# Kernel tuning notes

Measured on AMD Instinct MI355X. Metric: run time of the kernel, lower is better.

The kernel has to match this reference:

```python
import jax, jax.numpy as jnp
import numpy as np

NEG_SLOPE = 0.2


def gat_layer(x, W, a_src, a_dst, b, src, dst, num_nodes, heads, out_c, concat):
    # Linear transform per head: [N, heads, out_c]
    h = (x @ W).reshape(num_nodes, heads, out_c)
    # Per-node attention logits for source/dest roles: [N, heads]
    e_src = jnp.einsum('nhc,hc->nh', h, a_src)
    e_dst = jnp.einsum('nhc,hc->nh', h, a_dst)
    # Edge-wise scores (gather), LeakyReLU: [E, heads]
    e = jax.nn.leaky_relu(e_src[src] + e_dst[dst], negative_slope=NEG_SLOPE)
    # Segment softmax over incoming edges of each destination node
    m = jax.ops.segment_max(e, dst, num_segments=num_nodes)
    ex = jnp.exp(e - m[dst])
    denom = jax.ops.segment_sum(ex, dst, num_segments=num_nodes)
    alpha = ex / denom[dst]                       # [E, heads]
    # Weighted scatter-aggregate of source messages: [N, heads, out_c]
    out = jax.ops.segment_sum(h[src] * alpha[:, :, None], dst, num_segments=num_nodes)
    if concat:
        out = out.reshape(num_nodes, heads * out_c)
    else:
        out = out.mean(axis=1)
    return out + b


def setup_inputs() -> dict:
    key = jax.random.key(0)
    ks = jax.random.split(key, 12)
    N, E = 50000, 800000
    in_c, out_c, heads = 128, 32, 4
    x = jax.random.normal(ks[0], (N, in_c), dtype=jnp.float32)
    edge_index = jax.random.randint(ks[1], (2, E), 0, N, dtype=jnp.int64)
    s1 = 1.0 / np.sqrt(in_c)
    W1 = jax.random.normal(ks[2], (in_c, heads * out_c), dtype=jnp.float32) * s1
    a_src1 = jax.random.normal(ks[3], (heads, out_c), dtype=jnp.float32) * 0.1
    a_dst1 = jax.random.normal(ks[4], (heads, out_c), dtype=jnp.float32) * 0.1
    b1 = jnp.zeros((heads * out_c,), dtype=jnp.float32)
    s2 = 1.0 / np.sqrt(heads * out_c)
    W2 = jax.random.normal(ks[5], (heads * out_c, out_c), dtype=jnp.float32) * s2
    a_src2 = jax.random.normal(ks[6], (1, out_c), dtype=jnp.float32) * 0.1
    a_dst2 = jax.random.normal(ks[7], (1, out_c), dtype=jnp.float32) * 0.1
    b2 = jnp.zeros((out_c,), dtype=jnp.float32)
    return {"x": x, "edge_index": edge_index, "W1": W1, "a_src1": a_src1,
            "a_dst1": a_dst1, "b1": b1, "W2": W2, "a_src2": a_src2,
            "a_dst2": a_dst2, "b2": b2}


def reference(x, edge_index, W1, a_src1, a_dst1, b1, W2, a_src2, a_dst2, b2):
    N = x.shape[0]
    heads, out_c = a_src1.shape
    # add_self_loops=True (PyG default)
    loops = jnp.arange(N, dtype=edge_index.dtype)
    src = jnp.concatenate([edge_index[0], loops])
    dst = jnp.concatenate([edge_index[1], loops])
    h1 = gat_layer(x, W1, a_src1, a_dst1, b1, src, dst, N, heads, out_c, concat=True)
    h1 = jax.nn.elu(h1)
    out = gat_layer(h1, W2, a_src2, a_dst2, b2, src, dst, N, 1, out_c, concat=False)
    return out
```

## Files before the change

### kernel.cpp

```cpp
#include <hip/hip_runtime.h>
#include <hip/hip_bf16.h>

#define LRELU_SLOPE 0.2f
#define NB_SHIFT 7
#define NBLK 512

typedef __attribute__((ext_vector_type(8))) short short8;
typedef __attribute__((ext_vector_type(4))) float float4v;

__device__ inline float b2f(unsigned short u) {
    union { unsigned int i; float f; } v; v.i = ((unsigned int)u) << 16; return v.f;
}
__device__ inline unsigned short f2b(float f) {
    union { float f; unsigned int i; } v; v.f = f;
    unsigned int x = v.i;
    unsigned int r = x + 0x7fffu + ((x >> 16) & 1u);
    return (unsigned short)(r >> 16);
}
__device__ inline float lrelu(float x) { return x > 0.f ? x : LRELU_SLOPE * x; }

__global__ __launch_bounds__(256) void gemm1_mfma_kernel(
        const float* __restrict__ x, const float* __restrict__ W1,
        const float* __restrict__ a_src, const float* __restrict__ a_dst,
        unsigned short* __restrict__ h1b, float* __restrict__ es,
        float* __restrict__ ed, int N,
        const int* __restrict__ dst, int E, int Etot, int nb, int chunk,
        int* __restrict__ cnt) {
    __shared__ unsigned short xs[64][136];
    __shared__ unsigned short wt[128][136];
    int tid = threadIdx.x;
    int n0 = blockIdx.x * 64;

    for (int i = tid; i < 128 * 128; i += 256) {
        int k = i >> 7, n = i & 127;
        wt[n][k] = f2b(W1[i]);
    }
    {
        int rows = N - n0; if (rows > 64) rows = 64;
        const float4* xv = (const float4*)(x + (size_t)n0 * 128);
        int lim = rows * 32;
        for (int i = tid; i < lim; i += 256) {
            float4 v = xv[i];
            int r = i >> 5, c4 = (i & 31) << 2;
            uint2 p;
            p.x = (unsigned int)f2b(v.x) | ((unsigned int)f2b(v.y) << 16);
            p.y = (unsigned int)f2b(v.z) | ((unsigned int)f2b(v.w) << 16);
            *(uint2*)&xs[r][c4] = p;
        }
    }
    __syncthreads();

    int wave = tid >> 6;
    int lane = tid & 63;
    int lrow = lane & 15;
    int quad = lane >> 4;

    short8 afr[4];
#pragma unroll
    for (int kc = 0; kc < 4; kc++)
        afr[kc] = *(const short8*)&xs[wave * 16 + lrow][kc * 32 + quad * 8];
    __syncthreads();

#pragma unroll
    for (int ct = 0; ct < 8; ct++) {
        float4v acc = {0.f, 0.f, 0.f, 0.f};
#pragma unroll
        for (int kc = 0; kc < 4; kc++) {
            short8 bfr = *(const short8*)&wt[ct * 16 + lrow][kc * 32 + quad * 8];
            acc = __builtin_amdgcn_mfma_f32_16x16x32_bf16(afr[kc], bfr, acc, 0, 0, 0);
        }
#pragma unroll
        for (int r = 0; r < 4; r++) {
            int lr = wave * 16 + quad * 4 + r;
            int grow = n0 + lr;
            unsigned short hb = f2b(acc[r]);
            xs[lr][ct * 16 + lrow] = hb;
            if (grow < N)
                h1b[grow * 128 + ct * 16 + lrow] = hb;
        }
    }
    __syncthreads();

    int row = tid >> 2, h = tid & 3;
    int rg = n0 + row;
    if (rg < N) {
        const float* ap = a_src + h * 32;
        const float* bp = a_dst + h * 32;
        float s = 0.f, d = 0.f;
#pragma unroll
        for (int c2 = 0; c2 < 16; c2++) {
            unsigned int u = *(const unsigned int*)&xs[row][h * 32 + 2 * c2];
            float v0 = b2f((unsigned short)(u & 0xffffu));
            float v1 = b2f((unsigned short)(u >> 16));
            float2 a = *(const float2*)&ap[2 * c2];
            float2 b = *(const float2*)&bp[2 * c2];
            s += v0 * a.x + v1 * a.y;
            d += v0 * b.x + v1 * b.y;
        }
        es[rg * 4 + h] = s;
        ed[rg * 4 + h] = d;
    }

    int* histm = (int*)&wt[0][0];
    int blk = blockIdx.x;
    if (blk < NBLK)
        for (int i = tid; i < nb; i += 256) histm[i] = 0;
    __syncthreads();
    if (blk < NBLK) {
        int lo = blk * chunk;
        int hi = lo + chunk; if (hi > Etot) hi = Etot;
        for (int i = lo + tid; i < hi; i += 256) {
            int d = (i < E) ? dst[i] : (i - E);
            atomicAdd(&histm[d >> NB_SHIFT], 1);
        }
    }
    __syncthreads();
    if (blk < NBLK)
        for (int b = tid; b < nb; b += 256)
            cnt[b * NBLK + blk] = histm[b];
}

__global__ __launch_bounds__(1024) void scanA_kernel(int* cnt, int* bsum, int M) {
    __shared__ int tile[1024];
    int i = blockIdx.x * 1024 + threadIdx.x;
    int v = (i < M) ? cnt[i] : 0;
    tile[threadIdx.x] = v;
    __syncthreads();
    for (int off = 1; off < 1024; off <<= 1) {
        int t = (threadIdx.x >= (unsigned)off) ? tile[threadIdx.x - off] : 0;
        __syncthreads();
        tile[threadIdx.x] += t;
        __syncthreads();
    }
    int incl = tile[threadIdx.x];
    if (i < M) cnt[i] = incl - v;
    if (threadIdx.x == 1023) bsum[blockIdx.x] = incl;
}

__global__ __launch_bounds__(256) void scanB_kernel(int* __restrict__ bsum, int nb) {
    __shared__ int tile[256];
    int v = (threadIdx.x < (unsigned)nb) ? bsum[threadIdx.x] : 0;
    tile[threadIdx.x] = v;
    __syncthreads();
    for (int off = 1; off < 256; off <<= 1) {
        int t = (threadIdx.x >= (unsigned)off) ? tile[threadIdx.x - off] : 0;
        __syncthreads();
        tile[threadIdx.x] += t;
        __syncthreads();
    }
    if (threadIdx.x < (unsigned)nb) bsum[threadIdx.x] = tile[threadIdx.x] - v;
}

__global__ __launch_bounds__(256) void partition_kernel(
        const int* __restrict__ src, const int* __restrict__ dst,
        int E, int Etot, int nb, int chunk,
        const int* __restrict__ cnt, const int* __restrict__ boff,
        int2* __restrict__ bkt) {
    __shared__ int cur[512];
    int blk = blockIdx.x;
    for (int b = threadIdx.x; b < nb; b += 256) {
        int idx = b * NBLK + blk;
        cur[b] = cnt[idx] + boff[idx >> 10];
    }
    __syncthreads();
    int lo = blk * chunk;
    int hi = lo + chunk; if (hi > Etot) hi = Etot;
    for (int i = lo + threadIdx.x; i < hi; i += 256) {
        int s, d;
        if (i < E) { s = src[i]; d = dst[i]; }
        else       { s = d = i - E; }
        int pos = atomicAdd(&cur[d >> NB_SHIFT], 1);
        bkt[pos] = make_int2(s, d);
    }
}

__global__ __launch_bounds__(256) void finalize_kernel(
        const int2* __restrict__ bkt, const int* __restrict__ cnt,
        const int* __restrict__ boff, int nb,
        const float* __restrict__ es, const float* __restrict__ ed,
        int* __restrict__ ptr, int* __restrict__ csr_src,
        _Float16* __restrict__ w1h, int N, int Etot) {
    __shared__ int deg[128];
    __shared__ int scn[128];
    __shared__ int cur[128];
    int b = blockIdx.x;
    int idx0 = b * NBLK;
    int base = cnt[idx0] + boff[idx0 >> 10];
    int nextbase;
    if (b + 1 < nb) {
        int idx1 = (b + 1) * NBLK;
        nextbase = cnt[idx1] + boff[idx1 >> 10];
    } else nextbase = Etot;
    int count = nextbase - base;
    int node0 = b << NB_SHIFT;
    int nodes = N - node0; if (nodes > 128) nodes = 128;

    if (threadIdx.x < 128) deg[threadIdx.x] = 0;
    __syncthreads();
    for (int i = threadIdx.x; i < count; i += 256)
        atomicAdd(&deg[bkt[base + i].y - node0], 1);
    __syncthreads();
    int v = (threadIdx.x < 128) ? deg[threadIdx.x] : 0;
    if (threadIdx.x < 128) scn[threadIdx.x] = v;
    __syncthreads();
    for (int off = 1; off < 128; off <<= 1) {
        int t = (threadIdx.x < 128 && threadIdx.x >= (unsigned)off) ? scn[threadIdx.x - off] : 0;
        __syncthreads();
        if (threadIdx.x < 128) scn[threadIdx.x] += t;
        __syncthreads();
    }
    if (threadIdx.x < 128) {
        int excl = scn[threadIdx.x] - v;
        cur[threadIdx.x] = excl;
        if (threadIdx.x < nodes) ptr[node0 + threadIdx.x] = base + excl;
    }
    if (b == nb - 1 && threadIdx.x == 0) ptr[N] = Etot;
    __syncthreads();
    for (int i = threadIdx.x; i < count; i += 256) {
        int2 sd = bkt[base + i];
        int pos = base + atomicAdd(&cur[sd.y - node0], 1);
        csr_src[pos] = sd.x;
        float4 a = *(const float4*)&es[sd.x * 4];
        float4 bb = *(const float4*)&ed[sd.y * 4];
        union { _Float16 h[4]; uint2 u; } ww;
        ww.h[0] = (_Float16)__expf(lrelu(a.x + bb.x));
        ww.h[1] = (_Float16)__expf(lrelu(a.y + bb.y));
        ww.h[2] = (_Float16)__expf(lrelu(a.z + bb.z));
        ww.h[3] = (_Float16)__expf(lrelu(a.w + bb.w));
        *(uint2*)&w1h[(size_t)pos * 4] = ww.u;
    }
}

__global__ __launch_bounds__(256) void gemm2_mfma_kernel(
        const unsigned short* __restrict__ h1e, const float* __restrict__ W2,
        const float* __restrict__ a_src, const float* __restrict__ a_dst,
        unsigned short* __restrict__ h2b, float* __restrict__ es,
        float* __restrict__ ed, int N) {
    __shared__ unsigned short xs[64][136];
    __shared__ unsigned short wt[32][136];
    int tid = threadIdx.x;
    int n0 = blockIdx.x * 64;

    for (int i = tid; i < 128 * 32; i += 256) {
        int k = i >> 5, n = i & 31;
        wt[n][k] = f2b(W2[i]);
    }
    {
        const unsigned int* srcp = (const unsigned int*)(h1e + (size_t)n0 * 128);
        int rows = (N - n0) < 64 ? (N - n0) : 64;
        int maxu = rows * 64;
        for (int i = tid; i < 4096; i += 256) {
            unsigned int v = (i < maxu) ? srcp[i] : 0u;
            int r = i >> 6, cp = (i & 63) << 1;
            *(unsigned int*)&xs[r][cp] = v;
        }
    }
    __syncthreads();

    int wave = tid >> 6;
    int lane = tid & 63;
    int lrow = lane & 15;
    int quad = lane >> 4;

    short8 afr[4];
#pragma unroll
    for (int kc = 0; kc < 4; kc++)
        afr[kc] = *(const short8*)&xs[wave * 16 + lrow][kc * 32 + quad * 8];
    __syncthreads();

#pragma unroll
    for (int ct = 0; ct < 2; ct++) {
        float4v acc = {0.f, 0.f, 0.f, 0.f};
#pragma unroll
        for (int kc = 0; kc < 4; kc++) {
            short8 bfr = *(const short8*)&wt[ct * 16 + lrow][kc * 32 + quad * 8];
            acc = __builtin_amdgcn_mfma_f32_16x16x32_bf16(afr[kc], bfr, acc, 0, 0, 0);
        }
#pragma unroll
        for (int r = 0; r < 4; r++) {
            int lr = wave * 16 + quad * 4 + r;
            int grow = n0 + lr;
            unsigned short hb = f2b(acc[r]);
            xs[lr][ct * 16 + lrow] = hb;
            if (grow < N)
                h2b[(size_t)grow * 32 + ct * 16 + lrow] = hb;
        }
    }
    __syncthreads();

    if (tid < 64) {
        int rg = n0 + tid;
        if (rg < N) {
            float s = 0.f, d = 0.f;
#pragma unroll
            for (int c2 = 0; c2 < 16; c2++) {
                unsigned int u = *(const unsigned int*)&xs[tid][2 * c2];
                float v0 = b2f((unsigned short)(u & 0xffffu));
                float v1 = b2f((unsigned short)(u >> 16));
                float2 a = *(const float2*)&a_src[2 * c2];
                float2 b = *(const float2*)&a_dst[2 * c2];
                s += v0 * a.x + v1 * a.y;
                d += v0 * b.x + v1 * b.y;
            }
            es[rg] = s;
            ed[rg] = d;
        }
    }
}

__global__ __launch_bounds__(256) void agg1_kernel(
        const uint4* __restrict__ h1v, const _Float16* __restrict__ w1h,
        const int* __restrict__ csr, const int* __restrict__ ptr,
        const float* __restrict__ b1, uint4* __restrict__ h1e_v, int N) {
    int tid = threadIdx.x;
    int n = blockIdx.x * 16 + (tid >> 4);
    if (n >= N) return;
    int cl = tid & 15;
    int h = cl >> 2;
    int start = ptr[n], end = ptr[n + 1];
    float a0 = 0.f, a1 = 0.f, a2 = 0.f, a3 = 0.f;
    float a4 = 0.f, a5 = 0.f, a6 = 0.f, a7 = 0.f, ws = 0.f;
    int i = start;
    for (; i + 4 <= end; i += 4) {
        int s[4]; float v[4]; uint4 g[4];
#pragma unroll
        for (int k = 0; k < 4; k++) s[k] = csr[i + k];
#pragma unroll
        for (int k = 0; k < 4; k++) v[k] = (float)w1h[(size_t)(i + k) * 4 + h];
#pragma unroll
        for (int k = 0; k < 4; k++) g[k] = h1v[(s[k] << 4) + cl];
#pragma unroll
        for (int k = 0; k < 4; k++) {
            a0 += v[k] * b2f((unsigned short)(g[k].x & 0xffffu));
            a1 += v[k] * b2f((unsigned short)(g[k].x >> 16));
            a2 += v[k] * b2f((unsigned short)(g[k].y & 0xffffu));
            a3 += v[k] * b2f((unsigned short)(g[k].y >> 16));
            a4 += v[k] * b2f((unsigned short)(g[k].z & 0xffffu));
            a5 += v[k] * b2f((unsigned short)(g[k].z >> 16));
            a6 += v[k] * b2f((unsigned short)(g[k].w & 0xffffu));
            a7 += v[k] * b2f((unsigned short)(g[k].w >> 16));
            ws += v[k];
        }
    }
    for (; i < end; i++) {
        int s = csr[i];
        float v = (float)w1h[(size_t)i * 4 + h];
        uint4 g = h1v[(s << 4) + cl];
        a0 += v * b2f((unsigned short)(g.x & 0xffffu));
        a1 += v * b2f((unsigned short)(g.x >> 16));
        a2 += v * b2f((unsigned short)(g.y & 0xffffu));
        a3 += v * b2f((unsigned short)(g.y >> 16));
        a4 += v * b2f((unsigned short)(g.z & 0xffffu));
        a5 += v * b2f((unsigned short)(g.z >> 16));
        a6 += v * b2f((unsigned short)(g.w & 0xffffu));
        a7 += v * b2f((unsigned short)(g.w >> 16));
        ws += v;
    }
    float r = 1.f / ws;
    float4 bb0 = ((const float4*)b1)[cl * 2];
    float4 bb1 = ((const float4*)b1)[cl * 2 + 1];
    float o0 = a0 * r + bb0.x;
    float o1 = a1 * r + bb0.y;
    float o2 = a2 * r + bb0.z;
    float o3 = a3 * r + bb0.w;
    float o4 = a4 * r + bb1.x;
    float o5 = a5 * r + bb1.y;
    float o6 = a6 * r + bb1.z;
    float o7 = a7 * r + bb1.w;
    o0 = o0 > 0.f ? o0 : __expf(o0) - 1.f;
    o1 = o1 > 0.f ? o1 : __expf(o1) - 1.f;
    o2 = o2 > 0.f ? o2 : __expf(o2) - 1.f;
    o3 = o3 > 0.f ? o3 : __expf(o3) - 1.f;
    o4 = o4 > 0.f ? o4 : __expf(o4) - 1.f;
    o5 = o5 > 0.f ? o5 : __expf(o5) - 1.f;
    o6 = o6 > 0.f ? o6 : __expf(o6) - 1.f;
    o7 = o7 > 0.f ? o7 : __expf(o7) - 1.f;
    uint4 outv;
    outv.x = (unsigned int)f2b(o0) | ((unsigned int)f2b(o1) << 16);
    outv.y = (unsigned int)f2b(o2) | ((unsigned int)f2b(o3) << 16);
    outv.z = (unsigned int)f2b(o4) | ((unsigned int)f2b(o5) << 16);
    outv.w = (unsigned int)f2b(o6) | ((unsigned int)f2b(o7) << 16);
    h1e_v[(n << 4) + cl] = outv;
}

__global__ __launch_bounds__(256) void agg2_kernel(
        const uint2* __restrict__ h2v, const float* __restrict__ es,
        const float* __restrict__ ed, const int* __restrict__ csr,
        const int* __restrict__ ptr, const float* __restrict__ b2,
        float* __restrict__ out, int N) {
    int tid = threadIdx.x;
    int n = blockIdx.x * 32 + (tid >> 3);
    if (n >= N) return;
    int cl = tid & 7;
    float edl = ed[n];
    int start = ptr[n], end = ptr[n + 1];
    float a0 = 0.f, a1 = 0.f, a2 = 0.f, a3 = 0.f, ws = 0.f;
    int i = start;
    for (; i + 8 <= end; i += 8) {
        int s[8]; float e[8]; uint2 g[8];
#pragma unroll
        for (int k = 0; k < 8; k++) s[k] = csr[i + k];
#pragma unroll
        for (int k = 0; k < 8; k++) e[k] = es[s[k]];
#pragma unroll
        for (int k = 0; k < 8; k++) g[k] = h2v[(s[k] << 3) + cl];
#pragma unroll
        for (int k = 0; k < 8; k++) {
            float v = __expf(lrelu(e[k] + edl));
            a0 += v * b2f((unsigned short)(g[k].x & 0xffffu));
            a1 += v * b2f((unsigned short)(g[k].x >> 16));
            a2 += v * b2f((unsigned short)(g[k].y & 0xffffu));
            a3 += v * b2f((unsigned short)(g[k].y >> 16));
            ws += v;
        }
    }
    for (; i < end; i++) {
        int s = csr[i];
        float v = __expf(lrelu(es[s] + edl));
        uint2 g = h2v[(s << 3) + cl];
        a0 += v * b2f((unsigned short)(g.x & 0xffffu));
        a1 += v * b2f((unsigned short)(g.x >> 16));
        a2 += v * b2f((unsigned short)(g.y & 0xffffu));
        a3 += v * b2f((unsigned short)(g.y >> 16));
        ws += v;
    }
    float r = 1.f / ws;
    float4 bb = ((const float4*)b2)[cl];
    float4 o;
    o.x = a0 * r + bb.x;
    o.y = a1 * r + bb.y;
    o.z = a2 * r + bb.z;
    o.w = a3 * r + bb.w;
    ((float4*)out)[(size_t)n * 8 + cl] = o;
}

extern "C" void kernel_launch(void* const* d_in, const int* in_sizes, int n_in,
                              void* d_out, int out_size, void* d_ws, size_t ws_size,
                              hipStream_t stream) {
    const float* x      = (const float*)d_in[0];
    const int*   ei     = (const int*)  d_in[1];
    const float* W1     = (const float*)d_in[2];
    const float* a_src1 = (const float*)d_in[3];
    const float* a_dst1 = (const float*)d_in[4];
    const float* b1     = (const float*)d_in[5];
    const float* W2     = (const float*)d_in[6];
    const float* a_src2 = (const float*)d_in[7];
    const float* a_dst2 = (const float*)d_in[8];
    const float* b2     = (const float*)d_in[9];
    float* outp = (float*)d_out;

    const int N = in_sizes[0] / 128;
    const int E = in_sizes[1] / 2;
    const int Etot = E + N;

    const int* src = ei;
    const int* dst = ei + E;

    const int nb    = (N + 127) >> 7;
    const int chunk = (Etot + NBLK - 1) / NBLK;
    const int M = nb * NBLK;
    const int nbA = (M + 1023) / 1024;

    char* w = (char*)d_ws;
    unsigned short* h1b = (unsigned short*)(w + 0);
    unsigned short* h1e = (unsigned short*)(w + 12800000);
    unsigned short* h2b = (unsigned short*)(w + 25600000);
    float* es1  = (float*)(w + 28800000);
    float* ed1  = (float*)(w + 29600000);
    float* es2  = (float*)(w + 30400000);
    float* ed2  = (float*)(w + 30600000);
    int*   ptr  = (int*)  (w + 30800000);
    int*   bsum = (int*)  (w + 31000064);
    int*   cnt  = (int*)  (w + 31001088);
    int*   csr_src = (int*)(w + 31801856);
    int2*  bkt  = (int2*) (w + 35201856);
    _Float16* w1h = (_Float16*)(w + 42001856);

    gemm1_mfma_kernel<<<(N + 63) / 64, 256, 0, stream>>>(x, W1, a_src1, a_dst1,
                                                         h1b, es1, ed1, N,
                                                         dst, E, Etot, nb, chunk,
                                                         cnt);

    scanA_kernel<<<nbA, 1024, 0, stream>>>(cnt, bsum, M);
    scanB_kernel<<<1, 256, 0, stream>>>(bsum, nbA);
    partition_kernel<<<NBLK, 256, 0, stream>>>(src, dst, E, Etot, nb, chunk,
                                               cnt, bsum, bkt);
    finalize_kernel<<<nb, 256, 0, stream>>>(bkt, cnt, bsum, nb, es1, ed1,
                                            ptr, csr_src, w1h, N, Etot);

    agg1_kernel<<<(N + 15) / 16, 256, 0, stream>>>((const uint4*)h1b, w1h,
                                                   csr_src, ptr, b1,
                                                   (uint4*)h1e, N);

    gemm2_mfma_kernel<<<(N + 63) / 64, 256, 0, stream>>>(h1e, W2, a_src2, a_dst2,
                                                         h2b, es2, ed2, N);
    agg2_kernel<<<(N + 31) / 32, 256, 0, stream>>>((const uint2*)h2b, es2, ed2,
                                                   csr_src, ptr, b2, outp, N);
}
```

Measured before the change: 199.8 us.

## Assign one wavefront per node in aggregation kernels with edge-parallel lanes

Both aggregation kernels now give each destination node a full 64-lane wavefront. Lane groups process different edges in parallel and the partial sums are combined with cross-lane xor shuffles before one lane group writes the output. This is meant to raise memory-level parallelism for the gathers on high-degree nodes and cut per-thread serial edge loops. The cost is four times more blocks, wasted lanes on low-degree nodes, and the shuffle reduction. Separately, the W1 and W2 weight loads in both GEMM kernels are vectorized to float4 reads.

```diff
diff --git a/kernel.cpp b/kernel.cpp
--- a/kernel.cpp
+++ b/kernel.cpp
@@ -31,9 +31,16 @@
     int tid = threadIdx.x;
     int n0 = blockIdx.x * 64;
 
-    for (int i = tid; i < 128 * 128; i += 256) {
-        int k = i >> 7, n = i & 127;
-        wt[n][k] = f2b(W1[i]);
+    {
+        const float4* wv = (const float4*)W1;
+        for (int i = tid; i < 4096; i += 256) {
+            float4 v = wv[i];
+            int kk = i >> 5, n4 = (i & 31) << 2;
+            wt[n4 + 0][kk] = f2b(v.x);
+            wt[n4 + 1][kk] = f2b(v.y);
+            wt[n4 + 2][kk] = f2b(v.z);
+            wt[n4 + 3][kk] = f2b(v.w);
+        }
     }
     {
         int rows = N - n0; if (rows > 64) rows = 64;
@@ -241,9 +248,16 @@
     int tid = threadIdx.x;
     int n0 = blockIdx.x * 64;
 
-    for (int i = tid; i < 128 * 32; i += 256) {
-        int k = i >> 5, n = i & 31;
-        wt[n][k] = f2b(W2[i]);
+    {
+        const float4* wv = (const float4*)W2;
+        for (int i = tid; i < 1024; i += 256) {
+            float4 v = wv[i];
+            int kk = i >> 3, n4 = (i & 7) << 2;
+            wt[n4 + 0][kk] = f2b(v.x);
+            wt[n4 + 1][kk] = f2b(v.y);
+            wt[n4 + 2][kk] = f2b(v.z);
+            wt[n4 + 3][kk] = f2b(v.w);
+        }
     }
     {
         const unsigned int* srcp = (const unsigned int*)(h1e + (size_t)n0 * 128);
@@ -312,39 +326,49 @@
         const uint4* __restrict__ h1v, const _Float16* __restrict__ w1h,
         const int* __restrict__ csr, const int* __restrict__ ptr,
         const float* __restrict__ b1, uint4* __restrict__ h1e_v, int N) {
-    int tid = threadIdx.x;
-    int n = blockIdx.x * 16 + (tid >> 4);
+    int lane = threadIdx.x & 63;
+    int n = blockIdx.x * 4 + (threadIdx.x >> 6);
     if (n >= N) return;
-    int cl = tid & 15;
-    int h = cl >> 2;
+    int k  = lane >> 4;
+    int cl = lane & 15;
+    int h  = cl >> 2;
     int start = ptr[n], end = ptr[n + 1];
     float a0 = 0.f, a1 = 0.f, a2 = 0.f, a3 = 0.f;
     float a4 = 0.f, a5 = 0.f, a6 = 0.f, a7 = 0.f, ws = 0.f;
-    int i = start;
-    for (; i + 4 <= end; i += 4) {
-        int s[4]; float v[4]; uint4 g[4];
-#pragma unroll
-        for (int k = 0; k < 4; k++) s[k] = csr[i + k];
-#pragma unroll
-        for (int k = 0; k < 4; k++) v[k] = (float)w1h[(size_t)(i + k) * 4 + h];
-#pragma unroll
-        for (int k = 0; k < 4; k++) g[k] = h1v[(s[k] << 4) + cl];
-#pragma unroll
-        for (int k = 0; k < 4; k++) {
-            a0 += v[k] * b2f((unsigned short)(g[k].x & 0xffffu));
-            a1 += v[k] * b2f((unsigned short)(g[k].x >> 16));
-            a2 += v[k] * b2f((unsigned short)(g[k].y & 0xffffu));
-            a3 += v[k] * b2f((unsigned short)(g[k].y >> 16));
-            a4 += v[k] * b2f((unsigned short)(g[k].z & 0xffffu));
-            a5 += v[k] * b2f((unsigned short)(g[k].z >> 16));
-            a6 += v[k] * b2f((unsigned short)(g[k].w & 0xffffu));
-            a7 += v[k] * b2f((unsigned short)(g[k].w >> 16));
-            ws += v[k];
-        }
-    }
-    for (; i < end; i++) {
-        int s = csr[i];
-        float v = (float)w1h[(size_t)i * 4 + h];
+    int i0 = start;
+    for (; i0 + 8 <= end; i0 += 8) {
+        int iA = i0 + k, iB = iA + 4;
+        int sA = csr[iA];
+        int sB = csr[iB];
+        float vA = (float)w1h[iA * 4 + h];
+        float vB = (float)w1h[iB * 4 + h];
+        uint4 gA = h1v[(sA << 4) + cl];
+        uint4 gB = h1v[(sB << 4) + cl];
+        a0 += vA * b2f((unsigned short)(gA.x & 0xffffu));
+        a1 += vA * b2f((unsigned short)(gA.x >> 16));
+        a2 += vA * b2f((unsigned short)(gA.y & 0xffffu));
+        a3 += vA * b2f((unsigned short)(gA.y >> 16));
+        a4 += vA * b2f((unsigned short)(gA.z & 0xffffu));
+        a5 += vA * b2f((unsigned short)(gA.z >> 16));
+        a6 += vA * b2f((unsigned short)(gA.w & 0xffffu));
+        a7 += vA * b2f((unsigned short)(gA.w >> 16));
+        ws += vA;
+        a0 += vB * b2f((unsigned short)(gB.x & 0xffffu));
+        a1 += vB * b2f((unsigned short)(gB.x >> 16));
+        a2 += vB * b2f((unsigned short)(gB.y & 0xffffu));
+        a3 += vB * b2f((unsigned short)(gB.y >> 16));
+        a4 += vB * b2f((unsigned short)(gB.z & 0xffffu));
+        a5 += vB * b2f((unsigned short)(gB.z >> 16));
+        a6 += vB * b2f((unsigned short)(gB.w & 0xffffu));
+        a7 += vB * b2f((unsigned short)(gB.w >> 16));
+        ws += vB;
+    }
+    for (; i0 < end; i0 += 4) {
+        int idx = i0 + k;
+        bool ok = idx < end;
+        int idc = ok ? idx : end - 1;
+        int s = csr[idc];
+        float v = ok ? (float)w1h[idc * 4 + h] : 0.f;
         uint4 g = h1v[(s << 4) + cl];
         a0 += v * b2f((unsigned short)(g.x & 0xffffu));
         a1 += v * b2f((unsigned short)(g.x >> 16));
@@ -356,31 +380,42 @@
         a7 += v * b2f((unsigned short)(g.w >> 16));
         ws += v;
     }
-    float r = 1.f / ws;
-    float4 bb0 = ((const float4*)b1)[cl * 2];
-    float4 bb1 = ((const float4*)b1)[cl * 2 + 1];
-    float o0 = a0 * r + bb0.x;
-    float o1 = a1 * r + bb0.y;
-    float o2 = a2 * r + bb0.z;
-    float o3 = a3 * r + bb0.w;
-    float o4 = a4 * r + bb1.x;
-    float o5 = a5 * r + bb1.y;
-    float o6 = a6 * r + bb1.z;
-    float o7 = a7 * r + bb1.w;
-    o0 = o0 > 0.f ? o0 : __expf(o0) - 1.f;
-    o1 = o1 > 0.f ? o1 : __expf(o1) - 1.f;
-    o2 = o2 > 0.f ? o2 : __expf(o2) - 1.f;
-    o3 = o3 > 0.f ? o3 : __expf(o3) - 1.f;
-    o4 = o4 > 0.f ? o4 : __expf(o4) - 1.f;
-    o5 = o5 > 0.f ? o5 : __expf(o5) - 1.f;
-    o6 = o6 > 0.f ? o6 : __expf(o6) - 1.f;
-    o7 = o7 > 0.f ? o7 : __expf(o7) - 1.f;
-    uint4 outv;
-    outv.x = (unsigned int)f2b(o0) | ((unsigned int)f2b(o1) << 16);
-    outv.y = (unsigned int)f2b(o2) | ((unsigned int)f2b(o3) << 16);
-    outv.z = (unsigned int)f2b(o4) | ((unsigned int)f2b(o5) << 16);
-    outv.w = (unsigned int)f2b(o6) | ((unsigned int)f2b(o7) << 16);
-    h1e_v[(n << 4) + cl] = outv;
+    a0 += __shfl_xor(a0, 16); a0 += __shfl_xor(a0, 32);
+    a1 += __shfl_xor(a1, 16); a1 += __shfl_xor(a1, 32);
+    a2 += __shfl_xor(a2, 16); a2 += __shfl_xor(a2, 32);
+    a3 += __shfl_xor(a3, 16); a3 += __shfl_xor(a3, 32);
+    a4 += __shfl_xor(a4, 16); a4 += __shfl_xor(a4, 32);
+    a5 += __shfl_xor(a5, 16); a5 += __shfl_xor(a5, 32);
+    a6 += __shfl_xor(a6, 16); a6 += __shfl_xor(a6, 32);
+    a7 += __shfl_xor(a7, 16); a7 += __shfl_xor(a7, 32);
+    ws += __shfl_xor(ws, 16); ws += __shfl_xor(ws, 32);
+    if (k == 0) {
+        float r = 1.f / ws;
+        float4 bb0 = ((const float4*)b1)[cl * 2];
+        float4 bb1 = ((const float4*)b1)[cl * 2 + 1];
+        float o0 = a0 * r + bb0.x;
+        float o1 = a1 * r + bb0.y;
+        float o2 = a2 * r + bb0.z;
+        float o3 = a3 * r + bb0.w;
+        float o4 = a4 * r + bb1.x;
+        float o5 = a5 * r + bb1.y;
+        float o6 = a6 * r + bb1.z;
+        float o7 = a7 * r + bb1.w;
+        o0 = o0 > 0.f ? o0 : __expf(o0) - 1.f;
+        o1 = o1 > 0.f ? o1 : __expf(o1) - 1.f;
+        o2 = o2 > 0.f ? o2 : __expf(o2) - 1.f;
+        o3 = o3 > 0.f ? o3 : __expf(o3) - 1.f;
+        o4 = o4 > 0.f ? o4 : __expf(o4) - 1.f;
+        o5 = o5 > 0.f ? o5 : __expf(o5) - 1.f;
+        o6 = o6 > 0.f ? o6 : __expf(o6) - 1.f;
+        o7 = o7 > 0.f ? o7 : __expf(o7) - 1.f;
+        uint4 outv;
+        outv.x = (unsigned int)f2b(o0) | ((unsigned int)f2b(o1) << 16);
+        outv.y = (unsigned int)f2b(o2) | ((unsigned int)f2b(o3) << 16);
+        outv.z = (unsigned int)f2b(o4) | ((unsigned int)f2b(o5) << 16);
+        outv.w = (unsigned int)f2b(o6) | ((unsigned int)f2b(o7) << 16);
+        h1e_v[(n << 4) + cl] = outv;
+    }
 }
 
 __global__ __launch_bounds__(256) void agg2_kernel(
@@ -388,50 +423,65 @@
         const float* __restrict__ ed, const int* __restrict__ csr,
         const int* __restrict__ ptr, const float* __restrict__ b2,
         float* __restrict__ out, int N) {
-    int tid = threadIdx.x;
-    int n = blockIdx.x * 32 + (tid >> 3);
+    int lane = threadIdx.x & 63;
+    int n = blockIdx.x * 4 + (threadIdx.x >> 6);
     if (n >= N) return;
-    int cl = tid & 7;
+    int k  = lane >> 3;
+    int cl = lane & 7;
     float edl = ed[n];
     int start = ptr[n], end = ptr[n + 1];
     float a0 = 0.f, a1 = 0.f, a2 = 0.f, a3 = 0.f, ws = 0.f;
-    int i = start;
-    for (; i + 8 <= end; i += 8) {
-        int s[8]; float e[8]; uint2 g[8];
-#pragma unroll
-        for (int k = 0; k < 8; k++) s[k] = csr[i + k];
-#pragma unroll
-        for (int k = 0; k < 8; k++) e[k] = es[s[k]];
-#pragma unroll
-        for (int k = 0; k < 8; k++) g[k] = h2v[(s[k] << 3) + cl];
-#pragma unroll
-        for (int k = 0; k < 8; k++) {
-            float v = __expf(lrelu(e[k] + edl));
-            a0 += v * b2f((unsigned short)(g[k].x & 0xffffu));
-            a1 += v * b2f((unsigned short)(g[k].x >> 16));
-            a2 += v * b2f((unsigned short)(g[k].y & 0xffffu));
-            a3 += v * b2f((unsigned short)(g[k].y >> 16));
-            ws += v;
-        }
-    }
-    for (; i < end; i++) {
-        int s = csr[i];
-        float v = __expf(lrelu(es[s] + edl));
+    int i0 = start;
+    for (; i0 + 16 <= end; i0 += 16) {
+        int iA = i0 + k, iB = iA + 8;
+        int sA = csr[iA];
+        int sB = csr[iB];
+        float eA = es[sA];
+        float eB = es[sB];
+        uint2 gA = h2v[(sA << 3) + cl];
+        uint2 gB = h2v[(sB << 3) + cl];
+        float vA = __expf(lrelu(eA + edl));
+        float vB = __expf(lrelu(eB + edl));
+        a0 += vA * b2f((unsigned short)(gA.x & 0xffffu));
+        a1 += vA * b2f((unsigned short)(gA.x >> 16));
+        a2 += vA * b2f((unsigned short)(gA.y & 0xffffu));
+        a3 += vA * b2f((unsigned short)(gA.y >> 16));
+        ws += vA;
+        a0 += vB * b2f((unsigned short)(gB.x & 0xffffu));
+        a1 += vB * b2f((unsigned short)(gB.x >> 16));
+        a2 += vB * b2f((unsigned short)(gB.y & 0xffffu));
+        a3 += vB * b2f((unsigned short)(gB.y >> 16));
+        ws += vB;
+    }
+    for (; i0 < end; i0 += 8) {
+        int idx = i0 + k;
+        bool ok = idx < end;
+        int idc = ok ? idx : end - 1;
+        int s = csr[idc];
+        float e = es[s];
         uint2 g = h2v[(s << 3) + cl];
+        float v = ok ? __expf(lrelu(e + edl)) : 0.f;
         a0 += v * b2f((unsigned short)(g.x & 0xffffu));
         a1 += v * b2f((unsigned short)(g.x >> 16));
         a2 += v * b2f((unsigned short)(g.y & 0xffffu));
         a3 += v * b2f((unsigned short)(g.y >> 16));
         ws += v;
     }
-    float r = 1.f / ws;
-    float4 bb = ((const float4*)b2)[cl];
-    float4 o;
-    o.x = a0 * r + bb.x;
-    o.y = a1 * r + bb.y;
-    o.z = a2 * r + bb.z;
-    o.w = a3 * r + bb.w;
-    ((float4*)out)[(size_t)n * 8 + cl] = o;
+    a0 += __shfl_xor(a0, 8); a0 += __shfl_xor(a0, 16); a0 += __shfl_xor(a0, 32);
+    a1 += __shfl_xor(a1, 8); a1 += __shfl_xor(a1, 16); a1 += __shfl_xor(a1, 32);
+    a2 += __shfl_xor(a2, 8); a2 += __shfl_xor(a2, 16); a2 += __shfl_xor(a2, 32);
+    a3 += __shfl_xor(a3, 8); a3 += __shfl_xor(a3, 16); a3 += __shfl_xor(a3, 32);
+    ws += __shfl_xor(ws, 8); ws += __shfl_xor(ws, 16); ws += __shfl_xor(ws, 32);
+    if (k == 0) {
+        float r = 1.f / ws;
+        float4 bb = ((const float4*)b2)[cl];
+        float4 o;
+        o.x = a0 * r + bb.x;
+        o.y = a1 * r + bb.y;
+        o.z = a2 * r + bb.z;
+        o.w = a3 * r + bb.w;
+        ((float4*)out)[(size_t)n * 8 + cl] = o;
+    }
 }
 
 extern "C" void kernel_launch(void* const* d_in, const int* in_sizes, int n_in,
@@ -488,12 +538,12 @@
     finalize_kernel<<<nb, 256, 0, stream>>>(bkt, cnt, bsum, nb, es1, ed1,
                                             ptr, csr_src, w1h, N, Etot);
 
-    agg1_kernel<<<(N + 15) / 16, 256, 0, stream>>>((const uint4*)h1b, w1h,
-                                                   csr_src, ptr, b1,
-                                                   (uint4*)h1e, N);
+    agg1_kernel<<<(N + 3) / 4, 256, 0, stream>>>((const uint4*)h1b, w1h,
+                                                 csr_src, ptr, b1,
+                                                 (uint4*)h1e, N);
 
     gemm2_mfma_kernel<<<(N + 63) / 64, 256, 0, stream>>>(h1e, W2, a_src2, a_dst2,
                                                          h2b, es2, ed2, N);
-    agg2_kernel<<<(N + 31) / 32, 256, 0, stream>>>((const uint2*)h2b, es2, ed2,
-                                                   csr_src, ptr, b2, outp, N);
-}
+    agg2_kernel<<<(N + 3) / 4, 256, 0, stream>>>((const uint2*)h2b, es2, ed2,
+                                                 csr_src, ptr, b2, outp, N);
+}
```

Result: slower. 214.2 us (+7.2%).
